# Kernel optimization log

Hardware: AMD Instinct MI355X
Metric: run time of the kernel (lower is better)

Reference implementation:

```python
import jax, jax.numpy as jnp
import numpy as np

B, N, D = 16, 1024, 768
SCALE = D ** (-0.5)


def setup_inputs() -> dict:
    key = jax.random.key(0)
    ks = jax.random.split(key, 6)
    return {
        "x": jax.random.normal(ks[0], (B, N, D), dtype=jnp.float32),
        "y": jax.random.normal(ks[1], (B, N, D), dtype=jnp.float32),
        "coords": jax.random.normal(ks[2], (N, N, 6), dtype=jnp.float32),
        "W_qk": jax.random.normal(ks[3], (D, D), dtype=jnp.float32) * (D ** -0.5),
        "pos_emb": jax.random.normal(ks[4], (N, 6, 1), dtype=jnp.float32) * 0.02,
        "gating": jnp.float32(1.0),
        "temp": jnp.float32(0.1),
    }


def reference(x, y, coords, W_qk, pos_emb, gating, temp):
    # k = Linear(y), no bias; torch Linear: y @ W.T
    k = jnp.einsum('bnd,ed->bne', y, W_qk)
    # content score [B, N, N]
    patch_score = jax.nn.softmax(jnp.einsum('bnd,bmd->bnm', x, k) * SCALE, axis=-1)
    # positional score: coords [N, N, 6] @ pos_emb [N, 6, 1] -> [N, N]
    pos_score = jax.nn.softmax(jnp.einsum('pnk,pkl->pnl', coords, pos_emb)[..., 0], axis=-1)
    g = jax.nn.sigmoid(gating)
    attn = (1.0 - g) * patch_score + g * pos_score[None, :, :]  # broadcast over B
    out = jnp.einsum('bnm,bmd->bnd', attn, y)
    entropy = jnp.sum(-attn * jnp.log(attn + 1e-8), axis=-1, keepdims=True)  # [B, N, 1]
    hmap = 2.0 * (1.0 - jax.nn.sigmoid(temp * entropy))
    return out, hmap
```

## Files before the change

kernel.cpp:

```cpp
#include <hip/hip_runtime.h>
#include <hip/hip_bf16.h>
#include <cstdint>

typedef __bf16 bf16_t;
typedef __bf16 bf16x8 __attribute__((ext_vector_type(8)));
typedef __bf16 bf16x4 __attribute__((ext_vector_type(4)));
typedef float f32x4 __attribute__((ext_vector_type(4)));

static constexpr int B = 16, N = 1024, D = 768;
static constexpr float SCALE = 0.03608439182435161f;

#define ASYNC_COPY16(gptr, lptr)                                                          \
  __builtin_amdgcn_global_load_lds((const __attribute__((address_space(1))) void*)(gptr), \
                                   (__attribute__((address_space(3))) void*)(lptr), 16, 0, 0)

__device__ __forceinline__ float wave_red_max(float v) {
#pragma unroll
  for (int o = 32; o > 0; o >>= 1) v = fmaxf(v, __shfl_down(v, o, 64));
  return v;
}
__device__ __forceinline__ float wave_red_sum(float v) {
#pragma unroll
  for (int o = 32; o > 0; o >>= 1) v += __shfl_down(v, o, 64);
  return v;
}
__device__ __forceinline__ float block_max(float v, float* sm) {
  v = wave_red_max(v);
  int lane = threadIdx.x & 63, w = threadIdx.x >> 6;
  if (lane == 0) sm[w] = v;
  __syncthreads();
  return fmaxf(fmaxf(sm[0], sm[1]), fmaxf(sm[2], sm[3]));
}
__device__ __forceinline__ float block_sum(float v, float* sm) {
  v = wave_red_sum(v);
  int lane = threadIdx.x & 63, w = threadIdx.x >> 6;
  if (lane == 0) sm[w] = v;
  __syncthreads();
  return sm[0] + sm[1] + sm[2] + sm[3];
}

__global__ __launch_bounds__(256) void cast_f32_bf16_4(const float4* __restrict__ in,
                                                       bf16x4* __restrict__ out, int n4) {
  int i = blockIdx.x * 256 + threadIdx.x;
  if (i < n4) {
    float4 v = in[i];
    bf16x4 o;
    o.x = (bf16_t)v.x; o.y = (bf16_t)v.y; o.z = (bf16_t)v.z; o.w = (bf16_t)v.w;
    out[i] = o;
  }
}

__global__ __launch_bounds__(256) void transpose_bf16(const bf16_t* __restrict__ in,
                                                      bf16_t* __restrict__ out) {
  __shared__ bf16_t t[32][33];
  int b = blockIdx.z;
  int d0 = blockIdx.x * 32;
  int n0 = blockIdx.y * 32;
  int tx = threadIdx.x & 31;
  int ty = threadIdx.x >> 5;
  const bf16_t* src = in + (size_t)b * N * D;
  bf16_t* dst = out + (size_t)b * N * D;
#pragma unroll
  for (int r = 0; r < 4; r++) {
    int n = n0 + ty + r * 8;
    t[ty + r * 8][tx] = src[(size_t)n * D + d0 + tx];
  }
  __syncthreads();
#pragma unroll
  for (int r = 0; r < 4; r++) {
    int d = d0 + ty + r * 8;
    dst[(size_t)d * N + n0 + tx] = t[tx][ty + r * 8];
  }
}

__global__ __launch_bounds__(256) void pos_softmax_k(const float* __restrict__ coords,
                                                     const float* __restrict__ pemb,
                                                     float* __restrict__ pos) {
  __shared__ float sm1[4], sm2[4];
  int p = blockIdx.x;
  int tid = threadIdx.x;
  float e[6];
#pragma unroll
  for (int k = 0; k < 6; k++) e[k] = pemb[p * 6 + k];
  float v[4];
#pragma unroll
  for (int i = 0; i < 4; i++) {
    int n = tid + i * 256;
    const float* c = coords + ((size_t)p * N + n) * 6;
    float s = 0.f;
#pragma unroll
    for (int k = 0; k < 6; k++) s += c[k] * e[k];
    v[i] = s;
  }
  float m = block_max(fmaxf(fmaxf(v[0], v[1]), fmaxf(v[2], v[3])), sm1);
  float ex[4], ls = 0.f;
#pragma unroll
  for (int i = 0; i < 4; i++) { ex[i] = __expf(v[i] - m); ls += ex[i]; }
  float sum = block_sum(ls, sm2);
  float inv = 1.f / sum;
#pragma unroll
  for (int i = 0; i < 4; i++) pos[(size_t)p * N + tid + i * 256] = ex[i] * inv;
}

__global__ __launch_bounds__(256) void attn_entropy_k(float* __restrict__ S,
                                                      const float* __restrict__ pos,
                                                      const float* __restrict__ gating,
                                                      const float* __restrict__ temp,
                                                      float* __restrict__ hmap) {
  __shared__ float sm1[4], sm2[4], sm3[4];
  size_t row = blockIdx.x;
  int q = (int)(row & (size_t)(N - 1));
  int tid = threadIdx.x;
  float* Srow = S + row * N;
  float g = 1.f / (1.f + __expf(-gating[0]));
  float s[4];
#pragma unroll
  for (int i = 0; i < 4; i++) s[i] = Srow[tid + i * 256];
  float m = block_max(fmaxf(fmaxf(s[0], s[1]), fmaxf(s[2], s[3])), sm1);
  float e[4], ls = 0.f;
#pragma unroll
  for (int i = 0; i < 4; i++) { e[i] = __expf(s[i] - m); ls += e[i]; }
  float sum = block_sum(ls, sm2);
  float inv = 1.f / sum;
  const float* prow = pos + (size_t)q * N;
  float a[4], ent = 0.f;
#pragma unroll
  for (int i = 0; i < 4; i++) {
    float patch = e[i] * inv;
    float ps = prow[tid + i * 256];
    a[i] = (1.f - g) * patch + g * ps;
    ent += -a[i] * __logf(a[i] + 1e-8f);
  }
  float E = block_sum(ent, sm3);
  __syncthreads();
  bf16_t* arow = (bf16_t*)Srow;
#pragma unroll
  for (int i = 0; i < 4; i++) arow[tid + i * 256] = (bf16_t)a[i];
  if (tid == 0) hmap[row] = 2.f / (1.f + __expf(temp[0] * E));
}

template <typename OutT>
__global__ __launch_bounds__(256) void gemm_nt_128(const bf16_t* __restrict__ A, int lda, long long sA,
                                                   const bf16_t* __restrict__ Bm, int ldb, long long sB,
                                                   OutT* __restrict__ C, int ldc, long long sC,
                                                   int K, float scale) {
  __shared__ __align__(16) char lds_raw[4 * 32 * 68 * 4];
  bf16_t* As = (bf16_t*)lds_raw;
  bf16_t* Bs = (bf16_t*)(lds_raw + 16384);

  const int tid = threadIdx.x;
  const int lane = tid & 63, wave = tid >> 6;
  const int wr = wave >> 1, wc = wave & 1;
  const int quad = lane >> 4, lr = lane & 15;
  const int tileN = blockIdx.x * 128, tileM = blockIdx.y * 128;
  A += (long long)blockIdx.z * sA + (long long)tileM * lda;
  Bm += (long long)blockIdx.z * sB + (long long)tileN * ldb;
  C += (long long)blockIdx.z * sC;

  const bf16_t* ag = A + (long long)(wave * 32 + (lane >> 3)) * lda + (lane & 7) * 8;
  const bf16_t* bg = Bm + (long long)(wave * 32 + (lane >> 3)) * ldb + (lane & 7) * 8;

  f32x4 acc[4][4];
#pragma unroll
  for (int i = 0; i < 4; i++)
#pragma unroll
    for (int j = 0; j < 4; j++) acc[i][j] = (f32x4){0.f, 0.f, 0.f, 0.f};

  for (int kt = 0; kt < K; kt += 64) {
#pragma unroll
    for (int i = 0; i < 4; i++) {
      ASYNC_COPY16(ag + (long long)i * 8 * lda + kt, &As[(wave * 32 + i * 8) * 64]);
      ASYNC_COPY16(bg + (long long)i * 8 * ldb + kt, &Bs[(wave * 32 + i * 8) * 64]);
    }
    __syncthreads();
#pragma unroll
    for (int kk = 0; kk < 2; kk++) {
      bf16x8 af[4], bfr[4];
#pragma unroll
      for (int i = 0; i < 4; i++) {
        af[i] = *(const bf16x8*)&As[(wr * 64 + i * 16 + lr) * 64 + kk * 32 + quad * 8];
        bfr[i] = *(const bf16x8*)&Bs[(wc * 64 + i * 16 + lr) * 64 + kk * 32 + quad * 8];
      }
#pragma unroll
      for (int mi = 0; mi < 4; mi++)
#pragma unroll
        for (int nj = 0; nj < 4; nj++)
          acc[mi][nj] = __builtin_amdgcn_mfma_f32_16x16x32_bf16(af[mi], bfr[nj], acc[mi][nj], 0, 0, 0);
    }
    __syncthreads();
  }

  float* epi = (float*)lds_raw + wave * (32 * 68);
#pragma unroll
  for (int c = 0; c < 2; c++) {
#pragma unroll
    for (int m2 = 0; m2 < 2; m2++) {
      int mi = c * 2 + m2;
#pragma unroll
      for (int nj = 0; nj < 4; nj++)
#pragma unroll
        for (int r = 0; r < 4; r++) {
          int lrow = m2 * 16 + quad * 4 + r;
          epi[lrow * 68 + nj * 16 + lr] = acc[mi][nj][r] * scale;
        }
    }
    if constexpr (sizeof(OutT) == 4) {
#pragma unroll
      for (int seg = 0; seg < 8; seg++) {
        int lrow = seg * 4 + (lane >> 4);
        f32x4 v = *(const f32x4*)&epi[lrow * 68 + (lane & 15) * 4];
        long long grow = tileM + wr * 64 + c * 32 + lrow;
        int gcol = tileN + wc * 64 + (lane & 15) * 4;
        *(f32x4*)&C[grow * ldc + gcol] = v;
      }
    } else {
#pragma unroll
      for (int seg = 0; seg < 4; seg++) {
        int lrow = seg * 8 + (lane >> 3);
        const float* p = &epi[lrow * 68 + (lane & 7) * 8];
        f32x4 v0 = *(const f32x4*)&p[0];
        f32x4 v1 = *(const f32x4*)&p[4];
        bf16x8 o;
#pragma unroll
        for (int j = 0; j < 4; j++) { o[j] = (bf16_t)v0[j]; o[j + 4] = (bf16_t)v1[j]; }
        long long grow = tileM + wr * 64 + c * 32 + lrow;
        int gcol = tileN + wc * 64 + (lane & 7) * 8;
        *(bf16x8*)&C[grow * ldc + gcol] = o;
      }
    }
  }
}

extern "C" void kernel_launch(void* const* d_in, const int* in_sizes, int n_in,
                              void* d_out, int out_size, void* d_ws, size_t ws_size,
                              hipStream_t stream) {
  const float* x = (const float*)d_in[0];
  const float* y = (const float*)d_in[1];
  const float* coords = (const float*)d_in[2];
  const float* W = (const float*)d_in[3];
  const float* pemb = (const float*)d_in[4];
  const float* gating = (const float*)d_in[5];
  const float* temp = (const float*)d_in[6];
  float* out = (float*)d_out;
  float* hmap = out + (size_t)B * N * D;

  char* ws = (char*)d_ws;
  bf16_t* xb = (bf16_t*)(ws + 0);
  bf16_t* yb = (bf16_t*)(ws + 25165824);
  bf16_t* yT = (bf16_t*)(ws + 50331648);
  bf16_t* Wb = (bf16_t*)(ws + 75497472);
  bf16_t* kb = (bf16_t*)(ws + 76677120);
  float* pos = (float*)(ws + 101842944);
  float* S   = (float*)(ws + 106037248);

  const int BND = B * N * D;

  cast_f32_bf16_4<<<BND / 4 / 256, 256, 0, stream>>>((const float4*)x, (bf16x4*)xb, BND / 4);
  cast_f32_bf16_4<<<BND / 4 / 256, 256, 0, stream>>>((const float4*)y, (bf16x4*)yb, BND / 4);
  cast_f32_bf16_4<<<(D * D / 4 + 255) / 256, 256, 0, stream>>>((const float4*)W, (bf16x4*)Wb, D * D / 4);
  transpose_bf16<<<dim3(D / 32, N / 32, B), 256, 0, stream>>>(yb, yT);
  pos_softmax_k<<<N, 256, 0, stream>>>(coords, pemb, pos);

  gemm_nt_128<bf16_t><<<dim3(D / 128, (B * N) / 128, 1), 256, 0, stream>>>(
      yb, D, 0LL, Wb, D, 0LL, kb, D, 0LL, D, 1.0f);

  gemm_nt_128<float><<<dim3(N / 128, N / 128, B), 256, 0, stream>>>(
      xb, D, (long long)N * D, kb, D, (long long)N * D, S, N, (long long)N * N, D, SCALE);

  attn_entropy_k<<<B * N, 256, 0, stream>>>(S, pos, gating, temp, hmap);

  gemm_nt_128<float><<<dim3(D / 128, N / 128, B), 256, 0, stream>>>(
      (const bf16_t*)S, 2 * N, (long long)N * 2 * N, yT, N, (long long)N * D, out, D, (long long)N * D, N, 1.0f);
}
```

Baseline: 356.6 us.

## Enlarge GEMM tile to 256x128 with 8 waves and XCD-aware block swizzle

```diff
diff --git a/kernel.cpp b/kernel.cpp
--- a/kernel.cpp
+++ b/kernel.cpp
@@ -140,25 +140,38 @@
 }
 
 template <typename OutT>
-__global__ __launch_bounds__(256) void gemm_nt_128(const bf16_t* __restrict__ A, int lda, long long sA,
+__global__ __launch_bounds__(512) void gemm_nt_256(const bf16_t* __restrict__ A, int lda, long long sA,
                                                    const bf16_t* __restrict__ Bm, int ldb, long long sB,
                                                    OutT* __restrict__ C, int ldc, long long sC,
-                                                   int K, float scale) {
-  __shared__ __align__(16) char lds_raw[4 * 32 * 68 * 4];
+                                                   int K, float scale, int swz) {
+  __shared__ __align__(16) char lds_raw[49152];
   bf16_t* As = (bf16_t*)lds_raw;
-  bf16_t* Bs = (bf16_t*)(lds_raw + 16384);
+  bf16_t* Bs = (bf16_t*)(lds_raw + 32768);
 
   const int tid = threadIdx.x;
   const int lane = tid & 63, wave = tid >> 6;
   const int wr = wave >> 1, wc = wave & 1;
   const int quad = lane >> 4, lr = lane & 15;
-  const int tileN = blockIdx.x * 128, tileM = blockIdx.y * 128;
-  A += (long long)blockIdx.z * sA + (long long)tileM * lda;
-  Bm += (long long)blockIdx.z * sB + (long long)tileN * ldb;
-  C += (long long)blockIdx.z * sC;
+
+  int bx = blockIdx.x, by = blockIdx.y, bz = blockIdx.z;
+  if (swz) {
+    int Gx = gridDim.x, Gy = gridDim.y, Gz = gridDim.z;
+    int i = bx + Gx * (by + Gy * bz);
+    int xcd = i & 7, slot = i >> 3;
+    int T = Gx * Gy;
+    int bpx = Gz >> 3;
+    bz = xcd * bpx + slot / T;
+    int t = slot % T;
+    bx = t % Gx;
+    by = t / Gx;
+  }
+  const int tileN = bx * 128, tileM = by * 256;
+  A += (long long)bz * sA + (long long)tileM * lda;
+  Bm += (long long)bz * sB + (long long)tileN * ldb;
+  C += (long long)bz * sC;
 
   const bf16_t* ag = A + (long long)(wave * 32 + (lane >> 3)) * lda + (lane & 7) * 8;
-  const bf16_t* bg = Bm + (long long)(wave * 32 + (lane >> 3)) * ldb + (lane & 7) * 8;
+  const bf16_t* bg = Bm + (long long)(wave * 16 + (lane >> 3)) * ldb + (lane & 7) * 8;
 
   f32x4 acc[4][4];
 #pragma unroll
@@ -168,10 +181,11 @@
 
   for (int kt = 0; kt < K; kt += 64) {
 #pragma unroll
-    for (int i = 0; i < 4; i++) {
+    for (int i = 0; i < 4; i++)
       ASYNC_COPY16(ag + (long long)i * 8 * lda + kt, &As[(wave * 32 + i * 8) * 64]);
-      ASYNC_COPY16(bg + (long long)i * 8 * ldb + kt, &Bs[(wave * 32 + i * 8) * 64]);
-    }
+#pragma unroll
+    for (int i = 0; i < 2; i++)
+      ASYNC_COPY16(bg + (long long)i * 8 * ldb + kt, &Bs[(wave * 16 + i * 8) * 64]);
     __syncthreads();
 #pragma unroll
     for (int kk = 0; kk < 2; kk++) {
@@ -190,32 +204,26 @@
     __syncthreads();
   }
 
-  float* epi = (float*)lds_raw + wave * (32 * 68);
-#pragma unroll
-  for (int c = 0; c < 2; c++) {
-#pragma unroll
-    for (int m2 = 0; m2 < 2; m2++) {
-      int mi = c * 2 + m2;
-#pragma unroll
-      for (int nj = 0; nj < 4; nj++)
-#pragma unroll
-        for (int r = 0; r < 4; r++) {
-          int lrow = m2 * 16 + quad * 4 + r;
-          epi[lrow * 68 + nj * 16 + lr] = acc[mi][nj][r] * scale;
-        }
-    }
+  float* epi = (float*)lds_raw + wave * (16 * 68);
+#pragma unroll
+  for (int mi = 0; mi < 4; mi++) {
+#pragma unroll
+    for (int nj = 0; nj < 4; nj++)
+#pragma unroll
+      for (int r = 0; r < 4; r++)
+        epi[(quad * 4 + r) * 68 + nj * 16 + lr] = acc[mi][nj][r] * scale;
     if constexpr (sizeof(OutT) == 4) {
 #pragma unroll
-      for (int seg = 0; seg < 8; seg++) {
+      for (int seg = 0; seg < 4; seg++) {
         int lrow = seg * 4 + (lane >> 4);
         f32x4 v = *(const f32x4*)&epi[lrow * 68 + (lane & 15) * 4];
-        long long grow = tileM + wr * 64 + c * 32 + lrow;
+        long long grow = tileM + wr * 64 + mi * 16 + lrow;
         int gcol = tileN + wc * 64 + (lane & 15) * 4;
         *(f32x4*)&C[grow * ldc + gcol] = v;
       }
     } else {
 #pragma unroll
-      for (int seg = 0; seg < 4; seg++) {
+      for (int seg = 0; seg < 2; seg++) {
         int lrow = seg * 8 + (lane >> 3);
         const float* p = &epi[lrow * 68 + (lane & 7) * 8];
         f32x4 v0 = *(const f32x4*)&p[0];
@@ -223,7 +231,7 @@
         bf16x8 o;
 #pragma unroll
         for (int j = 0; j < 4; j++) { o[j] = (bf16_t)v0[j]; o[j + 4] = (bf16_t)v1[j]; }
-        long long grow = tileM + wr * 64 + c * 32 + lrow;
+        long long grow = tileM + wr * 64 + mi * 16 + lrow;
         int gcol = tileN + wc * 64 + (lane & 7) * 8;
         *(bf16x8*)&C[grow * ldc + gcol] = o;
       }
@@ -261,14 +269,14 @@
   transpose_bf16<<<dim3(D / 32, N / 32, B), 256, 0, stream>>>(yb, yT);
   pos_softmax_k<<<N, 256, 0, stream>>>(coords, pemb, pos);
 
-  gemm_nt_128<bf16_t><<<dim3(D / 128, (B * N) / 128, 1), 256, 0, stream>>>(
-      yb, D, 0LL, Wb, D, 0LL, kb, D, 0LL, D, 1.0f);
-
-  gemm_nt_128<float><<<dim3(N / 128, N / 128, B), 256, 0, stream>>>(
-      xb, D, (long long)N * D, kb, D, (long long)N * D, S, N, (long long)N * N, D, SCALE);
+  gemm_nt_256<bf16_t><<<dim3(D / 128, (B * N) / 256, 1), 512, 0, stream>>>(
+      yb, D, 0LL, Wb, D, 0LL, kb, D, 0LL, D, 1.0f, 0);
+
+  gemm_nt_256<float><<<dim3(N / 128, N / 256, B), 512, 0, stream>>>(
+      xb, D, (long long)N * D, kb, D, (long long)N * D, S, N, (long long)N * N, D, SCALE, 1);
 
   attn_entropy_k<<<B * N, 256, 0, stream>>>(S, pos, gating, temp, hmap);
 
-  gemm_nt_128<float><<<dim3(D / 128, N / 128, B), 256, 0, stream>>>(
-      (const bf16_t*)S, 2 * N, (long long)N * 2 * N, yT, N, (long long)N * D, out, D, (long long)N * D, N, 1.0f);
-}
+  gemm_nt_256<float><<<dim3(D / 128, N / 256, B), 512, 0, stream>>>(
+      (const bf16_t*)S, 2 * N, (long long)N * 2 * N, yT, N, (long long)N * D, out, D, (long long)N * D, N, 1.0f, 1);
+}
```

New measurement: 325.3 us. 1.1x faster.
